# Kernel optimization log

Measured on AMD Instinct MI355X. Metric: run time of the kernel, lower is better.

Reference implementation:

```python
import jax, jax.numpy as jnp
import numpy as np

B, S, D, H = 16, 577, 1280, 16
HD = D // H  # 80
HALF = HD // 2  # 40


def setup_inputs() -> dict:
    key = jax.random.key(0)
    ks = jax.random.split(key, 8)
    hidden_states = jax.random.normal(ks[0], (B, S, D), dtype=jnp.float32)
    # 2D rotary frequencies: random angles -> unit-magnitude complex rotations
    angles = jax.random.uniform(ks[1], (S, HALF), dtype=jnp.float32) * (2.0 * np.pi)
    freqs_cos = jnp.cos(angles)
    freqs_sin = jnp.sin(angles)
    scale = 1.0 / np.sqrt(D)
    Wq = jax.random.normal(ks[2], (D, D), dtype=jnp.float32) * scale
    Wk = jax.random.normal(ks[3], (D, D), dtype=jnp.float32) * scale
    Wv = jax.random.normal(ks[4], (D, D), dtype=jnp.float32) * scale
    Wo = jax.random.normal(ks[5], (D, D), dtype=jnp.float32) * scale
    z = jnp.zeros((D,), dtype=jnp.float32)
    return {
        "hidden_states": hidden_states,
        "freqs_cos": freqs_cos,
        "freqs_sin": freqs_sin,
        "Wq": Wq, "bq": z, "Wk": Wk, "bk": z,
        "Wv": Wv, "bv": z, "Wo": Wo, "bo": z,
    }


def _apply_rotary(x, cos, sin):
    # x: [B,S,H,HD]; cos/sin: [S, HD/2]; interleaved complex pairs (even=real, odd=imag)
    xr = x[..., 0::2]
    xi = x[..., 1::2]
    c = cos[None, :, None, :]
    s = sin[None, :, None, :]
    out_r = xr * c - xi * s
    out_i = xr * s + xi * c
    # re-interleave pairs back to [..., HD]
    return jnp.stack([out_r, out_i], axis=-1).reshape(x.shape)


def reference(hidden_states, freqs_cos, freqs_sin, Wq, bq, Wk, bk, Wv, bv, Wo, bo):
    q = (hidden_states @ Wq.T + bq).reshape(B, S, H, HD)
    k = (hidden_states @ Wk.T + bk).reshape(B, S, H, HD)
    v = (hidden_states @ Wv.T + bv).reshape(B, S, H, HD)
    q = _apply_rotary(q, freqs_cos, freqs_sin)
    k = _apply_rotary(k, freqs_cos, freqs_sin)
    # [B,H,S,HD]
    q = q.transpose(0, 2, 1, 3)
    k = k.transpose(0, 2, 1, 3)
    v = v.transpose(0, 2, 1, 3)
    scale = 1.0 / np.sqrt(HD).astype(np.float32)
    scores = jnp.einsum("bhsd,bhtd->bhst", q, k) * scale
    probs = jax.nn.softmax(scores, axis=-1)
    attn = jnp.einsum("bhst,bhtd->bhsd", probs, v)
    attn = attn.transpose(0, 2, 1, 3).reshape(B, S, D)
    return attn @ Wo.T + bo
```

## Files before the change

### kernel.cpp

```cpp
#include <hip/hip_runtime.h>

#define B_N 16
#define S_N 577
#define D_N 1280
#define H_N 16
#define HD_N 80
#define HALF_N 40
#define M_N 9232
#define M_PAD 9344
#define K_N 1280
#define VT_S 608
#define QSCALE 0.11180339887498949f

typedef __bf16 bf16_t;
typedef bf16_t bf16x8 __attribute__((ext_vector_type(8)));
typedef float f32x4 __attribute__((ext_vector_type(4)));

__device__ __forceinline__ float bf2f(unsigned short u) {
    union { unsigned int i; float f; } x; x.i = ((unsigned int)u) << 16; return x.f;
}
__device__ __forceinline__ unsigned short f2bf(float f) {
    union { unsigned int i; float f; } x; x.f = f;
    unsigned int r = x.i + 0x7FFFu + ((x.i >> 16) & 1u);
    return (unsigned short)(r >> 16);
}

__device__ __forceinline__ void gld_lds16(const unsigned short* g, unsigned short* l) {
    __builtin_amdgcn_global_load_lds(
        (const __attribute__((address_space(1))) unsigned int*)g,
        (__attribute__((address_space(3))) unsigned int*)l,
        16, 0, 0);
}

__global__ __launch_bounds__(256) void cvt_kernel(const float* __restrict__ in,
                                                  unsigned short* __restrict__ out, int n4) {
    int i = blockIdx.x * 256 + threadIdx.x;
    if (i < n4) {
        float4 v = ((const float4*)in)[i];
        ushort4 o;
        o.x = f2bf(v.x); o.y = f2bf(v.y); o.z = f2bf(v.z); o.w = f2bf(v.w);
        ((ushort4*)out)[i] = o;
    }
}

#define W4_N (D_N * K_N / 4)
__global__ __launch_bounds__(256) void cvt4_kernel(
    const float* __restrict__ w0, const float* __restrict__ w1,
    const float* __restrict__ w2, const float* __restrict__ w3,
    unsigned short* __restrict__ out) {
    int i = blockIdx.x * 256 + threadIdx.x;
    if (i >= 4 * W4_N) return;
    int r = i / W4_N, j = i - r * W4_N;
    const float* src = (r == 0) ? w0 : (r == 1) ? w1 : (r == 2) ? w2 : w3;
    float4 v = ((const float4*)src)[j];
    ushort4 o;
    o.x = f2bf(v.x); o.y = f2bf(v.y); o.z = f2bf(v.z); o.w = f2bf(v.w);
    ((ushort4*)out)[i] = o;
}

template <int MODE>
__global__ __launch_bounds__(256) void mgemm64_kernel(
    const unsigned short* __restrict__ A,
    const unsigned short* __restrict__ Wb,
    const float* __restrict__ b0, const float* __restrict__ b1,
    const float* __restrict__ b2,
    const float* __restrict__ cosb, const float* __restrict__ sinb,
    void* __restrict__ o0, void* __restrict__ o1, void* __restrict__ o2)
{
    __shared__ __align__(16) unsigned short As[2][128 * 64];
    __shared__ __align__(16) unsigned short Bs[2][128 * 64];

    const int tid = threadIdx.x;
    const int wave = tid >> 6, lane = tid & 63;
    const int quad = lane >> 4, n = lane & 15;
    const int wm = wave >> 1, wn = wave & 1;
    const int m0 = blockIdx.y * 128, n0g = blockIdx.x * 128;

    const int srow = lane >> 3;
    const int scol = (((lane & 7) ^ srow) * 8);

    const unsigned short* gA = A + (size_t)(m0 + wave * 32 + srow) * K_N + scol;
    const unsigned short* gB = Wb + (size_t)(n0g + wave * 32 + srow) * K_N + scol;
    const int lofs = wave * 32 * 64;

    f32x4 acc[4][4] = {};

    auto stage = [&](int pp, int k0) {
        unsigned short* lA = &As[pp][lofs];
        unsigned short* lB = &Bs[pp][lofs];
        #pragma unroll
        for (int i = 0; i < 4; ++i) {
            gld_lds16(gA + k0 + i * 8 * K_N, lA + i * 512);
            gld_lds16(gB + k0 + i * 8 * K_N, lB + i * 512);
        }
    };

    auto compute = [&](int pp) {
        #pragma unroll
        for (int kk = 0; kk < 2; ++kk) {
            const int sa = ((((kk << 2) | quad) ^ (n & 7)) * 8);
            bf16x8 af[4], bfr[4];
            #pragma unroll
            for (int mt = 0; mt < 4; ++mt)
                af[mt] = *(const bf16x8*)&As[pp][(wm * 64 + mt * 16 + n) * 64 + sa];
            #pragma unroll
            for (int nt = 0; nt < 4; ++nt)
                bfr[nt] = *(const bf16x8*)&Bs[pp][(wn * 64 + nt * 16 + n) * 64 + sa];
            #pragma unroll
            for (int mt = 0; mt < 4; ++mt)
                #pragma unroll
                for (int nt = 0; nt < 4; ++nt)
                    acc[mt][nt] = __builtin_amdgcn_mfma_f32_16x16x32_bf16(
                        af[mt], bfr[nt], acc[mt][nt], 0, 0, 0);
        }
    };

    stage(0, 0);

    #pragma unroll 2
    for (int t = 0; t < 19; ++t) {
        const int pp = t & 1;
        stage(pp ^ 1, (t + 1) * 64);
        asm volatile("s_waitcnt vmcnt(8)" ::: "memory");
        __builtin_amdgcn_s_barrier();
        compute(pp);
        __builtin_amdgcn_s_barrier();
    }
    asm volatile("s_waitcnt vmcnt(0)" ::: "memory");
    __builtin_amdgcn_s_barrier();
    compute(1);

    const int mbase = m0 + wm * 64;

    if (MODE == 3) {
        const int nbase = n0g + wn * 64;
        float* out = (float*)o0;
        #pragma unroll
        for (int mt = 0; mt < 4; ++mt)
            #pragma unroll
            for (int nt = 0; nt < 4; ++nt) {
                const int ncol = nbase + nt * 16 + n;
                const float bv = b0[ncol];
                #pragma unroll
                for (int r = 0; r < 4; ++r) {
                    int mrow = mbase + mt * 16 + quad * 4 + r;
                    if (mrow < M_N)
                        out[(size_t)mrow * D_N + ncol] = acc[mt][nt][r] + bv;
                }
            }
    } else {
        const int wsel = blockIdx.x / 10;
        const float* bias = (wsel == 0) ? b0 : (wsel == 1) ? b1 : b2;
        unsigned short* out =
            (unsigned short*)((wsel == 0) ? o0 : (wsel == 1) ? o1 : o2);
        const int nloc = n0g - wsel * 1280 + wn * 64;
        const bool evn = (n & 1) == 0;
        #pragma unroll
        for (int nt = 0; nt < 4; ++nt) {
            const int ncol = nloc + nt * 16 + n;
            const int h = ncol / HD_N, hd = ncol - h * HD_N;
            const float bv = bias[ncol];
            #pragma unroll
            for (int mt = 0; mt < 4; ++mt)
                #pragma unroll
                for (int r = 0; r < 4; ++r) {
                    int mrow = mbase + mt * 16 + quad * 4 + r;
                    int b = mrow / S_N, s = mrow - b * S_N;
                    float v = acc[mt][nt][r] + bv;
                    if (wsel == 2) {
                        if (mrow < M_N)
                            out[((size_t)(b * H_N + h) * HD_N + hd) * VT_S + s] =
                                f2bf(v);
                    } else {
                        float pv = __shfl_xor(v, 1);
                        float c  = cosb[s * HALF_N + (hd >> 1)];
                        float sn = sinb[s * HALF_N + (hd >> 1)];
                        float res = evn ? (v * c - pv * sn) : (pv * sn + v * c);
                        if (wsel == 0) res *= QSCALE;
                        if (mrow < M_N)
                            out[((size_t)(b * H_N + h) * S_N + s) * HD_N + hd] =
                                f2bf(res);
                    }
                }
        }
    }
}

__global__ __launch_bounds__(256) void fattn_kernel(
    const unsigned short* __restrict__ qb,
    const unsigned short* __restrict__ kb,
    const unsigned short* __restrict__ vt,
    unsigned short* __restrict__ attn)
{
    __shared__ __align__(16) unsigned short Plds[4][2][2][16 * 32];

    const int tid = threadIdx.x;
    const int wave = tid >> 6, lane = tid & 63;
    const int quad = lane >> 4, n = lane & 15;

    const int bid = blockIdx.x;
    const int xcd = bid & 7, t = bid >> 3;
    const int qt = t % 5, hl = t / 5;
    const int bh = hl * 8 + xcd;
    const int q0 = qt * 128 + wave * 32;

    const bf16x8 zf{};
    const unsigned short* qrow0 = qb + ((size_t)bh * S_N + q0 + n) * HD_N;
    const unsigned short* qrow1 = qrow0 + 16 * HD_N;
    bf16x8 aq00 = *(const bf16x8*)(qrow0 + quad * 8);
    bf16x8 aq01 = *(const bf16x8*)(qrow0 + 32 + quad * 8);
    bf16x8 aq02 = (quad < 2) ? *(const bf16x8*)(qrow0 + 64 + quad * 8) : zf;
    bf16x8 aq10 = *(const bf16x8*)(qrow1 + quad * 8);
    bf16x8 aq11 = *(const bf16x8*)(qrow1 + 32 + quad * 8);
    bf16x8 aq12 = (quad < 2) ? *(const bf16x8*)(qrow1 + 64 + quad * 8) : zf;

    const bf16_t one = (bf16_t)1.0f;
    const bf16x8 vones_all = {one, one, one, one, one, one, one, one};
    const bf16x8 vones = (n == 0) ? vones_all : zf;

    f32x4 o0[6] = {};
    f32x4 o1[6] = {};

    const unsigned short* kbase = kb + (size_t)bh * S_N * HD_N;
    const unsigned short* vbase = vt + (size_t)bh * HD_N * VT_S;

    #pragma unroll 2
    for (int t0 = 0; t0 < 608; t0 += 32) {
        const int pp = (t0 >> 5) & 1;
        unsigned short* pl0 = &Plds[wave][pp][0][0];
        unsigned short* pl1 = &Plds[wave][pp][1][0];

        const unsigned short* krA = kbase + (size_t)(t0 + n) * HD_N;
        const unsigned short* krB = krA + 16 * HD_N;
        bf16x8 bA0 = *(const bf16x8*)(krA + quad * 8);
        bf16x8 bA1 = *(const bf16x8*)(krA + 32 + quad * 8);
        bf16x8 bA2 = (quad < 2) ? *(const bf16x8*)(krA + 64 + quad * 8) : zf;
        bf16x8 bB0 = *(const bf16x8*)(krB + quad * 8);
        bf16x8 bB1 = *(const bf16x8*)(krB + 32 + quad * 8);
        bf16x8 bB2 = (quad < 2) ? *(const bf16x8*)(krB + 64 + quad * 8) : zf;

        f32x4 c00{}, c01{}, c10{}, c11{};
        c00 = __builtin_amdgcn_mfma_f32_16x16x32_bf16(aq00, bA0, c00, 0, 0, 0);
        c00 = __builtin_amdgcn_mfma_f32_16x16x32_bf16(aq01, bA1, c00, 0, 0, 0);
        c00 = __builtin_amdgcn_mfma_f32_16x16x32_bf16(aq02, bA2, c00, 0, 0, 0);
        c01 = __builtin_amdgcn_mfma_f32_16x16x32_bf16(aq00, bB0, c01, 0, 0, 0);
        c01 = __builtin_amdgcn_mfma_f32_16x16x32_bf16(aq01, bB1, c01, 0, 0, 0);
        c01 = __builtin_amdgcn_mfma_f32_16x16x32_bf16(aq02, bB2, c01, 0, 0, 0);
        c10 = __builtin_amdgcn_mfma_f32_16x16x32_bf16(aq10, bA0, c10, 0, 0, 0);
        c10 = __builtin_amdgcn_mfma_f32_16x16x32_bf16(aq11, bA1, c10, 0, 0, 0);
        c10 = __builtin_amdgcn_mfma_f32_16x16x32_bf16(aq12, bA2, c10, 0, 0, 0);
        c11 = __builtin_amdgcn_mfma_f32_16x16x32_bf16(aq10, bB0, c11, 0, 0, 0);
        c11 = __builtin_amdgcn_mfma_f32_16x16x32_bf16(aq11, bB1, c11, 0, 0, 0);
        c11 = __builtin_amdgcn_mfma_f32_16x16x32_bf16(aq12, bB2, c11, 0, 0, 0);

        const bool mA = (t0 + n) >= S_N;
        const bool mB = (t0 + 16 + n) >= S_N;

        #pragma unroll
        for (int r = 0; r < 4; ++r) {
            float p00 = mA ? 0.0f : __expf(c00[r]);
            float p01 = mB ? 0.0f : __expf(c01[r]);
            float p10 = mA ? 0.0f : __expf(c10[r]);
            float p11 = mB ? 0.0f : __expf(c11[r]);
            pl0[(quad * 4 + r) * 32 + n]      = f2bf(p00);
            pl0[(quad * 4 + r) * 32 + 16 + n] = f2bf(p01);
            pl1[(quad * 4 + r) * 32 + n]      = f2bf(p10);
            pl1[(quad * 4 + r) * 32 + 16 + n] = f2bf(p11);
        }

        bf16x8 ap0 = *(const bf16x8*)(pl0 + n * 32 + quad * 8);
        bf16x8 ap1 = *(const bf16x8*)(pl1 + n * 32 + quad * 8);

        #pragma unroll
        for (int nt = 0; nt < 5; ++nt) {
            const unsigned short* vr = vbase + (size_t)(nt * 16 + n) * VT_S + t0 + quad * 8;
            bf16x8 bv = *(const bf16x8*)vr;
            o0[nt] = __builtin_amdgcn_mfma_f32_16x16x32_bf16(ap0, bv, o0[nt], 0, 0, 0);
            o1[nt] = __builtin_amdgcn_mfma_f32_16x16x32_bf16(ap1, bv, o1[nt], 0, 0, 0);
        }
        o0[5] = __builtin_amdgcn_mfma_f32_16x16x32_bf16(ap0, vones, o0[5], 0, 0, 0);
        o1[5] = __builtin_amdgcn_mfma_f32_16x16x32_bf16(ap1, vones, o1[5], 0, 0, 0);
    }

    const int b = bh >> 4, h = bh & 15;
    #pragma unroll
    for (int r = 0; r < 4; ++r) {
        float l0 = __shfl(o0[5][r], lane & 48);
        float l1 = __shfl(o1[5][r], lane & 48);
        float linv0 = 1.0f / l0, linv1 = 1.0f / l1;
        int s0 = q0 + quad * 4 + r;
        int s1 = s0 + 16;
        #pragma unroll
        for (int nt = 0; nt < 5; ++nt) {
            if (s0 < S_N)
                attn[((size_t)b * S_N + s0) * D_N + h * HD_N + nt * 16 + n] =
                    f2bf(o0[nt][r] * linv0);
            if (s1 < S_N)
                attn[((size_t)b * S_N + s1) * D_N + h * HD_N + nt * 16 + n] =
                    f2bf(o1[nt][r] * linv1);
        }
    }
}

extern "C" void kernel_launch(void* const* d_in, const int* in_sizes, int n_in,
                              void* d_out, int out_size, void* d_ws, size_t ws_size,
                              hipStream_t stream) {
    const float* hs = (const float*)d_in[0];
    const float* fc = (const float*)d_in[1];
    const float* fs = (const float*)d_in[2];
    const float* Wq = (const float*)d_in[3];
    const float* bq = (const float*)d_in[4];
    const float* Wk = (const float*)d_in[5];
    const float* bk = (const float*)d_in[6];
    const float* Wv = (const float*)d_in[7];
    const float* bv = (const float*)d_in[8];
    const float* Wo = (const float*)d_in[9];
    const float* bo = (const float*)d_in[10];
    float* out = (float*)d_out;

    char* ws = (char*)d_ws;
    size_t off = 0;
    auto alloc = [&](size_t bytes) {
        char* p = ws + off; off += (bytes + 255) & ~(size_t)255; return p;
    };
    unsigned short* hsb  = (unsigned short*)alloc((size_t)M_PAD * K_N * 2);
    unsigned short* qb   = (unsigned short*)alloc((size_t)M_N * K_N * 2 + 32768);
    unsigned short* kb   = (unsigned short*)alloc((size_t)M_N * K_N * 2 + 32768);
    unsigned short* vt   = (unsigned short*)alloc((size_t)B_N * H_N * HD_N * VT_S * 2);
    unsigned short* Wall = (unsigned short*)alloc((size_t)4 * D_N * K_N * 2);

    const int HS4 = M_N * K_N / 4;
    dim3 blk(256);

    cvt_kernel<<<(HS4 + 255) / 256, blk, 0, stream>>>(hs, hsb, HS4);
    cvt4_kernel<<<(4 * W4_N + 255) / 256, blk, 0, stream>>>(Wq, Wk, Wv, Wo, Wall);

    mgemm64_kernel<4><<<dim3(30, 73), blk, 0, stream>>>(
        hsb, Wall, bq, bk, bv, fc, fs, qb, kb, vt);

    fattn_kernel<<<dim3(1280), blk, 0, stream>>>(qb, kb, vt, hsb );

    mgemm64_kernel<3><<<dim3(10, 73), blk, 0, stream>>>(
        hsb, Wall + 3 * (size_t)D_N * K_N, bo, bo, bo, fc, fs, out, out, out);
}
```

Before: 452.6 us.

## Replace QKV projection GEMM with 256x256-tile, 512-thread pipelined kernel

The fused QKV projection moves from a 128x128 tile, 256-thread kernel to a 256x256 tile, 8-wave kernel. It uses 128 KB of dynamic LDS, a four-stage half-K staging schedule, s_setprio around MFMA bursts and interleaved loads/barriers. The larger tile is meant to raise arithmetic intensity and cut global/LDS traffic per FLOP, and the new schedule overlaps loads with MFMAs. In exchange the grid becomes 15x37 blocks, which risks poorer wave quantization and occupancy on the GPU. The hidden-state buffer is padded further so the extra rows are covered.

```diff
diff --git a/kernel.cpp b/kernel.cpp
--- a/kernel.cpp
+++ b/kernel.cpp
@@ -8,6 +8,7 @@
 #define HALF_N 40
 #define M_N 9232
 #define M_PAD 9344
+#define M_PAD2 9472
 #define K_N 1280
 #define VT_S 608
 #define QSCALE 0.11180339887498949f
@@ -58,14 +59,152 @@
     ((ushort4*)out)[i] = o;
 }
 
-template <int MODE>
-__global__ __launch_bounds__(256) void mgemm64_kernel(
+#define PHASE_MFMA(AFR, BFR, MB) do {                                          \
+    __builtin_amdgcn_s_setprio(1);                                             \
+    _Pragma("unroll")                                                          \
+    for (int mf_ = 0; mf_ < 4; ++mf_) {                                        \
+        _Pragma("unroll")                                                      \
+        for (int nf_ = 0; nf_ < 4; ++nf_)                                      \
+            acc[(MB) + mf_][nf_] = __builtin_amdgcn_mfma_f32_16x16x32_bf16(    \
+                (AFR)[mf_], (BFR)[nf_], acc[(MB) + mf_][nf_], 0, 0, 0);        \
+    }                                                                          \
+    __builtin_amdgcn_s_setprio(0);                                             \
+} while (0)
+
+#define BARRIER() do {                                                         \
+    asm volatile("" ::: "memory");                                             \
+    __builtin_amdgcn_s_barrier();                                              \
+    __builtin_amdgcn_sched_barrier(0);                                         \
+    asm volatile("" ::: "memory");                                             \
+} while (0)
+
+#define VMCNT8() do { asm volatile("s_waitcnt vmcnt(8)" ::: "memory"); } while (0)
+
+#define KHALF(S, KK, ST_ODD, ST_EVEN) do {                                     \
+    bf16x8 bfr[4], af[4];                                                      \
+    _Pragma("unroll")                                                          \
+    for (int f_ = 0; f_ < 4; ++f_) bfr[f_] = rdB(S, KK, f_);                   \
+    _Pragma("unroll")                                                          \
+    for (int f_ = 0; f_ < 4; ++f_) af[f_] = rdA(S, KK, f_);                    \
+    ST_ODD;                                                                    \
+    PHASE_MFMA(af, bfr, 0);                                                    \
+    BARRIER();                                                                 \
+    _Pragma("unroll")                                                          \
+    for (int f_ = 0; f_ < 4; ++f_) af[f_] = rdA(S, KK, 4 + f_);                \
+    ST_EVEN;                                                                   \
+    PHASE_MFMA(af, bfr, 4);                                                    \
+    VMCNT8();                                                                  \
+    BARRIER();                                                                 \
+} while (0)
+
+__global__ __launch_bounds__(512, 2) void mgemm256_kernel(
     const unsigned short* __restrict__ A,
     const unsigned short* __restrict__ Wb,
     const float* __restrict__ b0, const float* __restrict__ b1,
     const float* __restrict__ b2,
     const float* __restrict__ cosb, const float* __restrict__ sinb,
     void* __restrict__ o0, void* __restrict__ o1, void* __restrict__ o2)
+{
+    extern __shared__ unsigned short smem[];
+    unsigned short* const Asb = smem;
+    unsigned short* const Bsb = smem + 4 * 8192;
+
+    const int tid = threadIdx.x;
+    const int wave = tid >> 6, lane = tid & 63;
+    const int quad = lane >> 4, n = lane & 15;
+    const int wm = wave >> 2, wn = wave & 3;
+    const int m0 = blockIdx.y * 256, n0g = blockIdx.x * 256;
+
+    const int srow = wave * 16 + (lane >> 2);
+    const int scb  = (lane & 3) ^ ((lane >> 2) & 3);
+
+    const unsigned short* gA = A  + (size_t)(m0  + srow) * K_N + scb * 8;
+    const unsigned short* gB = Wb + (size_t)(n0g + srow) * K_N + scb * 8;
+
+    f32x4 acc[8][4] = {};
+
+    auto stA = [&](int s, int h, int kt) {
+        unsigned short* l = Asb + (s * 2 + h) * 8192 + wave * 512;
+        const unsigned short* g = gA + kt * 64 + h * 32;
+        gld_lds16(g, l);
+        gld_lds16(g + (size_t)128 * K_N, l + 4096);
+    };
+    auto stB = [&](int s, int h, int kt) {
+        unsigned short* l = Bsb + (s * 2 + h) * 8192 + wave * 512;
+        const unsigned short* g = gB + kt * 64 + h * 32;
+        gld_lds16(g, l);
+        gld_lds16(g + (size_t)128 * K_N, l + 4096);
+    };
+
+    const int sa_blk = (quad ^ (n & 3)) * 8;
+    auto rdA = [&](int s, int kk, int mf) {
+        return *(const bf16x8*)&Asb[(s * 2 + kk) * 8192 +
+                                    (wm * 128 + mf * 16 + n) * 32 + sa_blk];
+    };
+    auto rdB = [&](int s, int kk, int nf) {
+        return *(const bf16x8*)&Bsb[(s * 2 + kk) * 8192 +
+                                    (wn * 64 + nf * 16 + n) * 32 + sa_blk];
+    };
+
+    stA(0, 0, 0); stB(0, 0, 0); stA(0, 1, 0); stB(0, 1, 0); stA(1, 0, 1); stB(1, 0, 1);
+    VMCNT8();
+    BARRIER();
+
+    #pragma unroll 1
+    for (int i = 0; i < 10; ++i) {
+        const int tb  = 2 * i + 1;
+        const int ta2 = (2 * i + 2 > 19) ? 19 : 2 * i + 2;
+        const int tb2 = (2 * i + 3 > 19) ? 19 : 2 * i + 3;
+        KHALF(0, 0, stA(1, 1, tb),  stB(1, 1, tb));
+        KHALF(0, 1, stA(0, 0, ta2), stB(0, 0, ta2));
+        KHALF(1, 0, stA(0, 1, ta2), stB(0, 1, ta2));
+        KHALF(1, 1, stA(1, 0, tb2), stB(1, 0, tb2));
+    }
+    asm volatile("s_waitcnt vmcnt(0)" ::: "memory");
+
+    const int wsel = blockIdx.x / 5;
+    const float* bias = (wsel == 0) ? b0 : (wsel == 1) ? b1 : b2;
+    unsigned short* out =
+        (unsigned short*)((wsel == 0) ? o0 : (wsel == 1) ? o1 : o2);
+    const int nloc0 = n0g - wsel * 1280 + wn * 64;
+    const bool evn = (n & 1) == 0;
+
+    #pragma unroll
+    for (int mf = 0; mf < 8; ++mf) {
+        #pragma unroll
+        for (int r = 0; r < 4; ++r) {
+            const int mrow = m0 + wm * 128 + mf * 16 + quad * 4 + r;
+            const int b = mrow / S_N, s = mrow - b * S_N;
+            const bool ok = mrow < M_N;
+            #pragma unroll
+            for (int nf = 0; nf < 4; ++nf) {
+                const int ncol = nloc0 + nf * 16 + n;
+                const int h = ncol / HD_N, hd = ncol - h * HD_N;
+                float v = acc[mf][nf][r] + bias[ncol];
+                if (wsel == 2) {
+                    if (ok)
+                        out[((size_t)(b * H_N + h) * HD_N + hd) * VT_S + s] = f2bf(v);
+                } else {
+                    float pv = __shfl_xor(v, 1);
+                    float c  = cosb[s * HALF_N + (hd >> 1)];
+                    float sn = sinb[s * HALF_N + (hd >> 1)];
+                    float res = evn ? (v * c - pv * sn) : (pv * sn + v * c);
+                    if (wsel == 0) res *= QSCALE;
+                    if (ok)
+                        out[((size_t)(b * H_N + h) * S_N + s) * HD_N + hd] = f2bf(res);
+                }
+            }
+        }
+    }
+}
+
+template <int MODE>
+__global__ __launch_bounds__(256) void mgemm64_kernel(
+    const unsigned short* __restrict__ A,
+    const unsigned short* __restrict__ Wb,
+    const float* __restrict__ b0,
+    const float* __restrict__ cosb, const float* __restrict__ sinb,
+    void* __restrict__ o0)
 {
     __shared__ __align__(16) unsigned short As[2][128 * 64];
     __shared__ __align__(16) unsigned short Bs[2][128 * 64];
@@ -131,59 +270,21 @@
     compute(1);
 
     const int mbase = m0 + wm * 64;
-
-    if (MODE == 3) {
-        const int nbase = n0g + wn * 64;
-        float* out = (float*)o0;
-        #pragma unroll
-        for (int mt = 0; mt < 4; ++mt)
+    const int nbase = n0g + wn * 64;
+    float* outp = (float*)o0;
+    #pragma unroll
+    for (int mt = 0; mt < 4; ++mt)
+        #pragma unroll
+        for (int nt = 0; nt < 4; ++nt) {
+            const int ncol = nbase + nt * 16 + n;
+            const float bv = b0[ncol];
             #pragma unroll
-            for (int nt = 0; nt < 4; ++nt) {
-                const int ncol = nbase + nt * 16 + n;
-                const float bv = b0[ncol];
-                #pragma unroll
-                for (int r = 0; r < 4; ++r) {
-                    int mrow = mbase + mt * 16 + quad * 4 + r;
-                    if (mrow < M_N)
-                        out[(size_t)mrow * D_N + ncol] = acc[mt][nt][r] + bv;
-                }
+            for (int r = 0; r < 4; ++r) {
+                int mrow = mbase + mt * 16 + quad * 4 + r;
+                if (mrow < M_N)
+                    outp[(size_t)mrow * D_N + ncol] = acc[mt][nt][r] + bv;
             }
-    } else {
-        const int wsel = blockIdx.x / 10;
-        const float* bias = (wsel == 0) ? b0 : (wsel == 1) ? b1 : b2;
-        unsigned short* out =
-            (unsigned short*)((wsel == 0) ? o0 : (wsel == 1) ? o1 : o2);
-        const int nloc = n0g - wsel * 1280 + wn * 64;
-        const bool evn = (n & 1) == 0;
-        #pragma unroll
-        for (int nt = 0; nt < 4; ++nt) {
-            const int ncol = nloc + nt * 16 + n;
-            const int h = ncol / HD_N, hd = ncol - h * HD_N;
-            const float bv = bias[ncol];
-            #pragma unroll
-            for (int mt = 0; mt < 4; ++mt)
-                #pragma unroll
-                for (int r = 0; r < 4; ++r) {
-                    int mrow = mbase + mt * 16 + quad * 4 + r;
-                    int b = mrow / S_N, s = mrow - b * S_N;
-                    float v = acc[mt][nt][r] + bv;
-                    if (wsel == 2) {
-                        if (mrow < M_N)
-                            out[((size_t)(b * H_N + h) * HD_N + hd) * VT_S + s] =
-                                f2bf(v);
-                    } else {
-                        float pv = __shfl_xor(v, 1);
-                        float c  = cosb[s * HALF_N + (hd >> 1)];
-                        float sn = sinb[s * HALF_N + (hd >> 1)];
-                        float res = evn ? (v * c - pv * sn) : (pv * sn + v * c);
-                        if (wsel == 0) res *= QSCALE;
-                        if (mrow < M_N)
-                            out[((size_t)(b * H_N + h) * S_N + s) * HD_N + hd] =
-                                f2bf(res);
-                    }
-                }
-        }
-    }
+        }
 }
 
 __global__ __launch_bounds__(256) void fattn_kernel(
@@ -323,7 +424,7 @@
     auto alloc = [&](size_t bytes) {
         char* p = ws + off; off += (bytes + 255) & ~(size_t)255; return p;
     };
-    unsigned short* hsb  = (unsigned short*)alloc((size_t)M_PAD * K_N * 2);
+    unsigned short* hsb  = (unsigned short*)alloc((size_t)M_PAD2 * K_N * 2);
     unsigned short* qb   = (unsigned short*)alloc((size_t)M_N * K_N * 2 + 32768);
     unsigned short* kb   = (unsigned short*)alloc((size_t)M_N * K_N * 2 + 32768);
     unsigned short* vt   = (unsigned short*)alloc((size_t)B_N * H_N * HD_N * VT_S * 2);
@@ -335,11 +436,13 @@
     cvt_kernel<<<(HS4 + 255) / 256, blk, 0, stream>>>(hs, hsb, HS4);
     cvt4_kernel<<<(4 * W4_N + 255) / 256, blk, 0, stream>>>(Wq, Wk, Wv, Wo, Wall);
 
-    mgemm64_kernel<4><<<dim3(30, 73), blk, 0, stream>>>(
+    (void)hipFuncSetAttribute(reinterpret_cast<const void*>(&mgemm256_kernel),
+                              hipFuncAttributeMaxDynamicSharedMemorySize, 131072);
+    mgemm256_kernel<<<dim3(15, 37), dim3(512), 131072, stream>>>(
         hsb, Wall, bq, bk, bv, fc, fs, qb, kb, vt);
 
     fattn_kernel<<<dim3(1280), blk, 0, stream>>>(qb, kb, vt, hsb );
 
     mgemm64_kernel<3><<<dim3(10, 73), blk, 0, stream>>>(
-        hsb, Wall + 3 * (size_t)D_N * K_N, bo, bo, bo, fc, fs, out, out, out);
-}
+        hsb, Wall + 3 * (size_t)D_N * K_N, bo, fc, fs, out);
+}
```

Result: slower. 467.6 us (+3.3%).

## Split QKV GEMM into dedicated kernel with 4-stage BK=32 pipeline

Applied to the files above, without the earlier changes.

Adds a separate QKV projection kernel that uses 32-wide K tiles with a four-deep LDS ring buffer and three tiles prefetched ahead, replacing the two-stage 64-wide K pipeline for that GEMM. The output projection keeps the original kernel, now specialized without the mode template. The aim is to hide global-load latency better for the largest GEMM, at the cost of more barriers per K and a different swizzle layout for the 32-wide tiles.

```diff
diff --git a/kernel.cpp b/kernel.cpp
--- a/kernel.cpp
+++ b/kernel.cpp
@@ -58,14 +58,111 @@
     ((ushort4*)out)[i] = o;
 }
 
-template <int MODE>
-__global__ __launch_bounds__(256) void mgemm64_kernel(
+__global__ __launch_bounds__(256) void qkv32_kernel(
     const unsigned short* __restrict__ A,
     const unsigned short* __restrict__ Wb,
     const float* __restrict__ b0, const float* __restrict__ b1,
     const float* __restrict__ b2,
     const float* __restrict__ cosb, const float* __restrict__ sinb,
     void* __restrict__ o0, void* __restrict__ o1, void* __restrict__ o2)
+{
+    __shared__ __align__(16) unsigned short As[4][128 * 32];
+    __shared__ __align__(16) unsigned short Bs[4][128 * 32];
+
+    const int tid = threadIdx.x;
+    const int wave = tid >> 6, lane = tid & 63;
+    const int quad = lane >> 4, n = lane & 15;
+    const int wm = wave >> 1, wn = wave & 1;
+    const int m0 = blockIdx.y * 128, n0g = blockIdx.x * 128;
+
+    const int scb = (lane & 3) ^ ((lane >> 3) & 3);
+
+    const unsigned short* gA = A + (size_t)(m0 + wave * 32 + (lane >> 2)) * K_N + scb * 8;
+    const unsigned short* gB = Wb + (size_t)(n0g + wave * 32 + (lane >> 2)) * K_N + scb * 8;
+
+    f32x4 acc[4][4] = {};
+
+    auto stage = [&](int s, int kt) {
+        unsigned short* lA = &As[s][wave * 1024];
+        unsigned short* lB = &Bs[s][wave * 1024];
+        const unsigned short* a = gA + kt * 32;
+        const unsigned short* b = gB + kt * 32;
+        gld_lds16(a, lA);
+        gld_lds16(a + 16 * K_N, lA + 512);
+        gld_lds16(b, lB);
+        gld_lds16(b + 16 * K_N, lB + 512);
+    };
+
+    const int sa_blk = (quad ^ ((n >> 1) & 3)) * 8;
+    auto compute = [&](int s) {
+        bf16x8 af[4], bfr[4];
+        #pragma unroll
+        for (int nt = 0; nt < 4; ++nt)
+            bfr[nt] = *(const bf16x8*)&Bs[s][(wn * 64 + nt * 16 + n) * 32 + sa_blk];
+        #pragma unroll
+        for (int mt = 0; mt < 4; ++mt)
+            af[mt] = *(const bf16x8*)&As[s][(wm * 64 + mt * 16 + n) * 32 + sa_blk];
+        #pragma unroll
+        for (int mt = 0; mt < 4; ++mt)
+            #pragma unroll
+            for (int nt = 0; nt < 4; ++nt)
+                acc[mt][nt] = __builtin_amdgcn_mfma_f32_16x16x32_bf16(
+                    af[mt], bfr[nt], acc[mt][nt], 0, 0, 0);
+    };
+
+    stage(0, 0); stage(1, 1); stage(2, 2);
+
+    #pragma unroll 4
+    for (int t = 0; t < 40; ++t) {
+        const int tn = (t + 3 < 40) ? t + 3 : 39;
+        stage((t + 3) & 3, tn);
+        asm volatile("s_waitcnt vmcnt(12)" ::: "memory");
+        __builtin_amdgcn_s_barrier();
+        compute(t & 3);
+        __builtin_amdgcn_s_barrier();
+    }
+    asm volatile("s_waitcnt vmcnt(0)" ::: "memory");
+
+    const int mbase = m0 + wm * 64;
+    const int wsel = blockIdx.x / 10;
+    const float* bias = (wsel == 0) ? b0 : (wsel == 1) ? b1 : b2;
+    unsigned short* out =
+        (unsigned short*)((wsel == 0) ? o0 : (wsel == 1) ? o1 : o2);
+    const int nloc = n0g - wsel * 1280 + wn * 64;
+    const bool evn = (n & 1) == 0;
+    #pragma unroll
+    for (int nt = 0; nt < 4; ++nt) {
+        const int ncol = nloc + nt * 16 + n;
+        const int h = ncol / HD_N, hd = ncol - h * HD_N;
+        const float bv = bias[ncol];
+        #pragma unroll
+        for (int mt = 0; mt < 4; ++mt)
+            #pragma unroll
+            for (int r = 0; r < 4; ++r) {
+                int mrow = mbase + mt * 16 + quad * 4 + r;
+                int b = mrow / S_N, s = mrow - b * S_N;
+                float v = acc[mt][nt][r] + bv;
+                if (wsel == 2) {
+                    if (mrow < M_N)
+                        out[((size_t)(b * H_N + h) * HD_N + hd) * VT_S + s] = f2bf(v);
+                } else {
+                    float pv = __shfl_xor(v, 1);
+                    float c  = cosb[s * HALF_N + (hd >> 1)];
+                    float sn = sinb[s * HALF_N + (hd >> 1)];
+                    float res = evn ? (v * c - pv * sn) : (pv * sn + v * c);
+                    if (wsel == 0) res *= QSCALE;
+                    if (mrow < M_N)
+                        out[((size_t)(b * H_N + h) * S_N + s) * HD_N + hd] = f2bf(res);
+                }
+            }
+    }
+}
+
+__global__ __launch_bounds__(256) void mgemm64_kernel(
+    const unsigned short* __restrict__ A,
+    const unsigned short* __restrict__ Wb,
+    const float* __restrict__ b0,
+    void* __restrict__ o0)
 {
     __shared__ __align__(16) unsigned short As[2][128 * 64];
     __shared__ __align__(16) unsigned short Bs[2][128 * 64];
@@ -131,59 +228,21 @@
     compute(1);
 
     const int mbase = m0 + wm * 64;
-
-    if (MODE == 3) {
-        const int nbase = n0g + wn * 64;
-        float* out = (float*)o0;
-        #pragma unroll
-        for (int mt = 0; mt < 4; ++mt)
-            #pragma unroll
-            for (int nt = 0; nt < 4; ++nt) {
-                const int ncol = nbase + nt * 16 + n;
-                const float bv = b0[ncol];
-                #pragma unroll
-                for (int r = 0; r < 4; ++r) {
-                    int mrow = mbase + mt * 16 + quad * 4 + r;
-                    if (mrow < M_N)
-                        out[(size_t)mrow * D_N + ncol] = acc[mt][nt][r] + bv;
-                }
+    const int nbase = n0g + wn * 64;
+    float* outp = (float*)o0;
+    #pragma unroll
+    for (int mt = 0; mt < 4; ++mt)
+        #pragma unroll
+        for (int nt = 0; nt < 4; ++nt) {
+            const int ncol = nbase + nt * 16 + n;
+            const float bv = b0[ncol];
+            #pragma unroll
+            for (int r = 0; r < 4; ++r) {
+                int mrow = mbase + mt * 16 + quad * 4 + r;
+                if (mrow < M_N)
+                    outp[(size_t)mrow * D_N + ncol] = acc[mt][nt][r] + bv;
             }
-    } else {
-        const int wsel = blockIdx.x / 10;
-        const float* bias = (wsel == 0) ? b0 : (wsel == 1) ? b1 : b2;
-        unsigned short* out =
-            (unsigned short*)((wsel == 0) ? o0 : (wsel == 1) ? o1 : o2);
-        const int nloc = n0g - wsel * 1280 + wn * 64;
-        const bool evn = (n & 1) == 0;
-        #pragma unroll
-        for (int nt = 0; nt < 4; ++nt) {
-            const int ncol = nloc + nt * 16 + n;
-            const int h = ncol / HD_N, hd = ncol - h * HD_N;
-            const float bv = bias[ncol];
-            #pragma unroll
-            for (int mt = 0; mt < 4; ++mt)
-                #pragma unroll
-                for (int r = 0; r < 4; ++r) {
-                    int mrow = mbase + mt * 16 + quad * 4 + r;
-                    int b = mrow / S_N, s = mrow - b * S_N;
-                    float v = acc[mt][nt][r] + bv;
-                    if (wsel == 2) {
-                        if (mrow < M_N)
-                            out[((size_t)(b * H_N + h) * HD_N + hd) * VT_S + s] =
-                                f2bf(v);
-                    } else {
-                        float pv = __shfl_xor(v, 1);
-                        float c  = cosb[s * HALF_N + (hd >> 1)];
-                        float sn = sinb[s * HALF_N + (hd >> 1)];
-                        float res = evn ? (v * c - pv * sn) : (pv * sn + v * c);
-                        if (wsel == 0) res *= QSCALE;
-                        if (mrow < M_N)
-                            out[((size_t)(b * H_N + h) * S_N + s) * HD_N + hd] =
-                                f2bf(res);
-                    }
-                }
-        }
-    }
+        }
 }
 
 __global__ __launch_bounds__(256) void fattn_kernel(
@@ -335,11 +394,11 @@
     cvt_kernel<<<(HS4 + 255) / 256, blk, 0, stream>>>(hs, hsb, HS4);
     cvt4_kernel<<<(4 * W4_N + 255) / 256, blk, 0, stream>>>(Wq, Wk, Wv, Wo, Wall);
 
-    mgemm64_kernel<4><<<dim3(30, 73), blk, 0, stream>>>(
+    qkv32_kernel<<<dim3(30, 73), blk, 0, stream>>>(
         hsb, Wall, bq, bk, bv, fc, fs, qb, kb, vt);
 
     fattn_kernel<<<dim3(1280), blk, 0, stream>>>(qb, kb, vt, hsb );
 
-    mgemm64_kernel<3><<<dim3(10, 73), blk, 0, stream>>>(
-        hsb, Wall + 3 * (size_t)D_N * K_N, bo, bo, bo, fc, fs, out, out, out);
-}
+    mgemm64_kernel<<<dim3(10, 73), blk, 0, stream>>>(
+        hsb, Wall + 3 * (size_t)D_N * K_N, bo, out);
+}
```

Result: slower. 479.7 us (+6.0%).
